# Kernel optimization log

Measured on AMD Instinct MI355X. Metric: run time of the kernel, lower is better.

The kernel has to match this reference:

```python
import jax, jax.numpy as jnp
import numpy as np

N_NODES = 100000
N_EDGES = 1600000
F_IN, HID, N_CLS = 64, 64, 40


def setup_inputs() -> dict:
    key = jax.random.key(0)
    ks = jax.random.split(key, 8)
    feats = jax.random.normal(ks[0], (N_NODES, F_IN), dtype=jnp.float32)
    src = jax.random.randint(ks[1], (N_EDGES,), 0, N_NODES, dtype=jnp.int32)
    dst = jax.random.randint(ks[2], (N_EDGES,), 0, N_NODES, dtype=jnp.int32)
    def lin(k, out_d, in_d):
        s = 1.0 / np.sqrt(in_d)
        return jax.random.uniform(k, (out_d, in_d), jnp.float32, -s, s)
    return {
        "features": feats,
        "src": src,
        "dst": dst,
        "W0": lin(ks[3], HID, F_IN), "b0": jnp.zeros((HID,), jnp.float32),
        "W1": lin(ks[4], HID, HID), "b1": jnp.zeros((HID,), jnp.float32),
        "W2": lin(ks[5], N_CLS, HID), "b2": jnp.zeros((N_CLS,), jnp.float32),
    }


def reference(features, src, dst, W0, b0, W1, b1, W2, b2):
    n = features.shape[0]
    # in-degrees (gcn aggregator normalizes by deg + 1, counting self-loop)
    deg = jax.ops.segment_sum(jnp.ones_like(dst, dtype=features.dtype), dst,
                              num_segments=n)  # [N]
    inv = 1.0 / (deg + 1.0)  # [N]

    def sage_gcn(h, W, b, act):
        # gather src features, sum into dst: message passing
        neigh = jax.ops.segment_sum(h[src], dst, num_segments=n)  # [N, d]
        h_neigh = (neigh + h) * inv[:, None]
        out = h_neigh @ W.T + b
        return jax.nn.relu(out) if act else out

    h = sage_gcn(features, W0, b0, True)
    h = sage_gcn(h, W1, b1, True)   # dropout = identity in eval mode
    h = sage_gcn(h, W2, b2, False)
    return h
```

## Files before the change

kernel.cpp:

```cpp
#include <hip/hip_runtime.h>
#include <hip/hip_bf16.h>


#define N_FEAT 64
#define CAP 64
#define CAPW 24
#define OVF_CAP 4096

__device__ __forceinline__ float rl(float v, int l) {
    return __int_as_float(__builtin_amdgcn_readlane(__float_as_int(v), l));
}

__device__ __forceinline__ void bin_body(const int* __restrict__ src,
                                         const int* __restrict__ dst,
                                         unsigned int* __restrict__ bins,
                                         unsigned long long* __restrict__ cnt64,
                                         int* __restrict__ ovf, int* __restrict__ ovf_cnt,
                                         int n_edges, int bsize, int nw, int bid) {
    const int e = bid * 256 + threadIdx.x;
    const int lane = threadIdx.x & 63;
    const int wid = (bid << 2) | (threadIdx.x >> 6);
    const bool valid = e < n_edges;
    int s = 0, d = 0;
    if (valid) { s = src[e]; d = dst[e]; }
    const unsigned int bucket = valid ? ((unsigned int)d / (unsigned int)bsize) : 8u;
    const unsigned int local = valid ? (unsigned int)(d - (int)bucket * bsize) : 0u;
    const unsigned int pack = (local << 17) | (unsigned int)s;

    int mycnt = 0;
    for (int c = 0; c < 8; ++c) {
        unsigned long long m = __ballot(valid && bucket == (unsigned int)c);
        int cc = __popcll(m);
        if (lane == c) mycnt = (cc < CAPW) ? cc : CAPW;
        if (valid && bucket == (unsigned int)c) {
            int pfx = __popcll(m & ((1ull << lane) - 1ull));
            if (pfx < CAPW) {
                __builtin_nontemporal_store(pack, &bins[((size_t)c * nw + wid) * CAPW + pfx]);
            } else {
                int p = atomicAdd(ovf_cnt, 1);
                if (p < OVF_CAP) { ovf[2 * p] = s; ovf[2 * p + 1] = d; }
            }
        }
    }
    unsigned long long packed = 0;
#pragma unroll
    for (int c = 0; c < 8; ++c) {
        int v = __builtin_amdgcn_readlane(mycnt, c);
        packed |= ((unsigned long long)(v & 0xFF)) << (8 * c);
    }
    if (lane == 0) cnt64[wid] = packed;
}

__device__ __forceinline__ void transform64_body(const float* __restrict__ h,
                                                 const float* __restrict__ W,
                                                 float* __restrict__ t, int n_nodes, int bid) {
    const int lane = threadIdx.x & 63;
    const int wave = (bid << 2) | (threadIdx.x >> 6);
    float4 wreg[16];
    const float4* W4 = (const float4*)(W + lane * N_FEAT);
#pragma unroll
    for (int k = 0; k < 16; ++k) wreg[k] = W4[k];
    const float* wf = (const float*)wreg;

    const int node0 = wave * 8;
    for (int k = 0; k < 8; ++k) {
        const int node = node0 + k;
        if (node >= n_nodes) return;
        const float hv = h[(size_t)node * N_FEAT + lane];
        float acc = 0.f;
#pragma unroll
        for (int f = 0; f < 64; ++f) acc = fmaf(rl(hv, f), wf[f], acc);
        t[(size_t)node * N_FEAT + lane] = acc;
    }
}

__global__ __launch_bounds__(256) void prep(const int* __restrict__ src,
                                            const int* __restrict__ dst,
                                            unsigned int* __restrict__ bins,
                                            unsigned long long* __restrict__ cnt64,
                                            int* __restrict__ ovf, int* __restrict__ ovf_cnt,
                                            int n_edges, int bsize, int nw,
                                            const float* __restrict__ feats,
                                            const float* __restrict__ W0,
                                            float* __restrict__ t0, int n_nodes, int PB) {
    const int b = (int)blockIdx.x;
    if (b < PB)
        bin_body(src, dst, bins, cnt64, ovf, ovf_cnt, n_edges, bsize, nw, b);
    else
        transform64_body(feats, W0, t0, n_nodes, b - PB);
}

__global__ __launch_bounds__(256) void fill_from_bins(const unsigned int* __restrict__ bins,
                                                      const unsigned long long* __restrict__ cnt64,
                                                      const int* __restrict__ ovf,
                                                      const int* __restrict__ ovf_cnt,
                                                      int* __restrict__ deg,
                                                      int* __restrict__ ell,
                                                      int nw, int bsize, int n_nodes) {
    const int lane = threadIdx.x & 63;
    const int w = threadIdx.x >> 6;
    const int c = blockIdx.x & 7;
    const int jb = blockIdx.x >> 3;
    const int base_node = c * bsize;
    const int sub = lane >> 3;
    const int rr = lane & 7;
    const int wave_in_bucket = jb * 4 + w;
    const int nwaves = (gridDim.x >> 3) * 4;
    const int shift = 8 * c;

    for (int s0 = wave_in_bucket * 8; s0 < nw; s0 += nwaves * 8) {
        const int sg = s0 + sub;
        unsigned long long word = (sg < nw) ? cnt64[sg] : 0ull;
        const int n = (int)((word >> shift) & 0xFFull);
#pragma unroll
        for (int t = 0; t < 3; ++t) {
            const int rec = t * 8 + rr;
            const bool act = rec < n;
            unsigned long long bm = __ballot(act);
            if (!bm) break;
            if (act) {
                unsigned int v = __builtin_nontemporal_load(
                    &bins[((size_t)c * nw + sg) * CAPW + rec]);
                int sv = (int)(v & 0x1FFFFu);
                int d = base_node + (int)(v >> 17);
                int slot = atomicAdd(&deg[d], 1);
                if (slot < CAP)
                    ell[(((size_t)(slot >> 4) * n_nodes + d) << 4) + (slot & 15)] = sv;
            }
        }
    }
    if (blockIdx.x == 0) {
        int n = *ovf_cnt; n = (n < OVF_CAP) ? n : OVF_CAP;
        for (int i = threadIdx.x; i < n; i += 256) {
            int sv = ovf[2 * i], d = ovf[2 * i + 1];
            int slot = atomicAdd(&deg[d], 1);
            if (slot < CAP)
                ell[(((size_t)(slot >> 4) * n_nodes + d) << 4) + (slot & 15)] = sv;
        }
    }
}

template <int OUTW, int NPW>
__global__ __launch_bounds__(256, 4) void agg_t_k(const float* __restrict__ t,
                                                  const float* __restrict__ bias,
                                                  const float* __restrict__ Wn,
                                                  const int* __restrict__ deg,
                                                  const int* __restrict__ ell,
                                                  float* __restrict__ tn,
                                                  int n_nodes) {
    __shared__ float4 sW[64 * 17];
    {
        const float4* Wg = (const float4*)Wn;
        for (int i = threadIdx.x; i < OUTW * 16; i += 256)
            sW[(i >> 4) * 17 + (i & 15)] = Wg[i];
    }
    __syncthreads();

    const int lane = threadIdx.x & 63;
    const int wave = (blockIdx.x << 2) | (threadIdx.x >> 6);
    const int g = lane >> 4;
    const int q = lane & 15;
    const float4* t4 = (const float4*)t;
    const int4* ell4 = (const int4*)ell;
    const float4 bq = ((const float4*)bias)[q];
    const int wrow = (OUTW == 64) ? lane : ((lane < OUTW) ? lane : 0);
    const float4* wrow4 = sW + wrow * 17;
    const bool has_out = (OUTW == 64) || (lane < OUTW);

    const int node0 = wave * NPW;
    if (node0 >= n_nodes) return;
    const int e0 = g * 4;

    if (node0 + NPW <= n_nodes) {
        int dg[NPW];
#pragma unroll
        for (int k = 0; k < NPW; ++k) dg[k] = deg[node0 + k];
        float4 self[NPW];
#pragma unroll
        for (int k = 0; k < NPW; ++k) self[k] = t4[(size_t)(node0 + k) * 16 + q];

        int4 idxb[2];
        float4 vb[2][4];
        idxb[0] = ell4[(size_t)node0 * 4 + g];
        {
            int4 ix = idxb[0]; const int d = dg[0];
            vb[0][0] = t4[(size_t)((e0 + 0 < d) ? ix.x : 0) * 16 + q];
            vb[0][1] = t4[(size_t)((e0 + 1 < d) ? ix.y : 0) * 16 + q];
            vb[0][2] = t4[(size_t)((e0 + 2 < d) ? ix.z : 0) * 16 + q];
            vb[0][3] = t4[(size_t)((e0 + 3 < d) ? ix.w : 0) * 16 + q];
        }
        if (NPW > 1) idxb[1] = ell4[(size_t)(node0 + 1) * 4 + g];

#pragma unroll
        for (int k = 0; k < NPW; ++k) {
            if (k + 1 < NPW) {
                int4 ix = idxb[(k + 1) & 1]; const int d = dg[k + 1];
                float4* v = vb[(k + 1) & 1];
                v[0] = t4[(size_t)((e0 + 0 < d) ? ix.x : 0) * 16 + q];
                v[1] = t4[(size_t)((e0 + 1 < d) ? ix.y : 0) * 16 + q];
                v[2] = t4[(size_t)((e0 + 2 < d) ? ix.z : 0) * 16 + q];
                v[3] = t4[(size_t)((e0 + 3 < d) ? ix.w : 0) * 16 + q];
            }
            if (k + 2 < NPW) idxb[k & 1] = ell4[(size_t)(node0 + k + 2) * 4 + g];

            const int node = node0 + k;
            const int d = dg[k];
            const float4* v = vb[k & 1];
            const float m0 = (e0 + 0 < d) ? 1.f : 0.f;
            const float m1 = (e0 + 1 < d) ? 1.f : 0.f;
            const float m2 = (e0 + 2 < d) ? 1.f : 0.f;
            const float m3 = (e0 + 3 < d) ? 1.f : 0.f;
            float4 acc;
            acc.x = m0 * v[0].x; acc.y = m0 * v[0].y; acc.z = m0 * v[0].z; acc.w = m0 * v[0].w;
            acc.x = fmaf(m1, v[1].x, acc.x); acc.y = fmaf(m1, v[1].y, acc.y);
            acc.z = fmaf(m1, v[1].z, acc.z); acc.w = fmaf(m1, v[1].w, acc.w);
            acc.x = fmaf(m2, v[2].x, acc.x); acc.y = fmaf(m2, v[2].y, acc.y);
            acc.z = fmaf(m2, v[2].z, acc.z); acc.w = fmaf(m2, v[2].w, acc.w);
            acc.x = fmaf(m3, v[3].x, acc.x); acc.y = fmaf(m3, v[3].y, acc.y);
            acc.z = fmaf(m3, v[3].z, acc.z); acc.w = fmaf(m3, v[3].w, acc.w);

            const int dcap = (d < CAP) ? d : CAP;
            for (int u = 1; u * 16 < dcap; ++u) {
                int4 ix = ell4[((size_t)u * n_nodes + node) * 4 + g];
                const int eb = u * 16 + g * 4;
                int i0 = (eb + 0 < d) ? ix.x : 0;
                int i1 = (eb + 1 < d) ? ix.y : 0;
                int i2 = (eb + 2 < d) ? ix.z : 0;
                int i3 = (eb + 3 < d) ? ix.w : 0;
                float n0 = (eb + 0 < d) ? 1.f : 0.f;
                float n1 = (eb + 1 < d) ? 1.f : 0.f;
                float n2 = (eb + 2 < d) ? 1.f : 0.f;
                float n3 = (eb + 3 < d) ? 1.f : 0.f;
                float4 w0 = t4[(size_t)i0 * 16 + q];
                float4 w1 = t4[(size_t)i1 * 16 + q];
                float4 w2 = t4[(size_t)i2 * 16 + q];
                float4 w3 = t4[(size_t)i3 * 16 + q];
                acc.x = fmaf(n0, w0.x, acc.x); acc.y = fmaf(n0, w0.y, acc.y);
                acc.z = fmaf(n0, w0.z, acc.z); acc.w = fmaf(n0, w0.w, acc.w);
                acc.x = fmaf(n1, w1.x, acc.x); acc.y = fmaf(n1, w1.y, acc.y);
                acc.z = fmaf(n1, w1.z, acc.z); acc.w = fmaf(n1, w1.w, acc.w);
                acc.x = fmaf(n2, w2.x, acc.x); acc.y = fmaf(n2, w2.y, acc.y);
                acc.z = fmaf(n2, w2.z, acc.z); acc.w = fmaf(n2, w2.w, acc.w);
                acc.x = fmaf(n3, w3.x, acc.x); acc.y = fmaf(n3, w3.y, acc.y);
                acc.z = fmaf(n3, w3.z, acc.z); acc.w = fmaf(n3, w3.w, acc.w);
            }

            acc.x += __shfl_xor(acc.x, 16, 64); acc.y += __shfl_xor(acc.y, 16, 64);
            acc.z += __shfl_xor(acc.z, 16, 64); acc.w += __shfl_xor(acc.w, 16, 64);
            acc.x += __shfl_xor(acc.x, 32, 64); acc.y += __shfl_xor(acc.y, 32, 64);
            acc.z += __shfl_xor(acc.z, 32, 64); acc.w += __shfl_xor(acc.w, 32, 64);

            const float invv = 1.0f / (float)(d + 1);
            float4 r;
            r.x = fmaxf((acc.x + self[k].x) * invv + bq.x, 0.f);
            r.y = fmaxf((acc.y + self[k].y) * invv + bq.y, 0.f);
            r.z = fmaxf((acc.z + self[k].z) * invv + bq.z, 0.f);
            r.w = fmaxf((acc.w + self[k].w) * invv + bq.w, 0.f);

            float o0 = 0.f, o1 = 0.f;
#pragma unroll
            for (int c = 0; c < 16; c += 2) {
                float4 w0 = wrow4[c];
                float4 w1 = wrow4[c + 1];
                o0 = fmaf(rl(r.x, c), w0.x, o0);
                o0 = fmaf(rl(r.y, c), w0.y, o0);
                o0 = fmaf(rl(r.z, c), w0.z, o0);
                o0 = fmaf(rl(r.w, c), w0.w, o0);
                o1 = fmaf(rl(r.x, c + 1), w1.x, o1);
                o1 = fmaf(rl(r.y, c + 1), w1.y, o1);
                o1 = fmaf(rl(r.z, c + 1), w1.z, o1);
                o1 = fmaf(rl(r.w, c + 1), w1.w, o1);
            }
            if (has_out) tn[(size_t)node * OUTW + lane] = o0 + o1;
        }
    } else {
        for (int k = 0; k < NPW; ++k) {
            const int node = node0 + k;
            if (node >= n_nodes) return;
            const int d = deg[node];
            const int dcap = (d < CAP) ? d : CAP;
            float4 acc = make_float4(0.f, 0.f, 0.f, 0.f);
            for (int u = 0; u * 16 < dcap; ++u) {
                int4 ix = ell4[((size_t)u * n_nodes + node) * 4 + g];
                const int eb = u * 16 + g * 4;
                for (int j = 0; j < 4; ++j) {
                    int ii = (j == 0) ? ix.x : (j == 1) ? ix.y : (j == 2) ? ix.z : ix.w;
                    float mm = (eb + j < d) ? 1.f : 0.f;
                    if (eb + j >= d) ii = 0;
                    float4 vv = t4[(size_t)ii * 16 + q];
                    acc.x = fmaf(mm, vv.x, acc.x); acc.y = fmaf(mm, vv.y, acc.y);
                    acc.z = fmaf(mm, vv.z, acc.z); acc.w = fmaf(mm, vv.w, acc.w);
                }
            }
            acc.x += __shfl_xor(acc.x, 16, 64); acc.y += __shfl_xor(acc.y, 16, 64);
            acc.z += __shfl_xor(acc.z, 16, 64); acc.w += __shfl_xor(acc.w, 16, 64);
            acc.x += __shfl_xor(acc.x, 32, 64); acc.y += __shfl_xor(acc.y, 32, 64);
            acc.z += __shfl_xor(acc.z, 32, 64); acc.w += __shfl_xor(acc.w, 32, 64);
            float4 self = t4[(size_t)node * 16 + q];
            const float invv = 1.0f / (float)(d + 1);
            float4 r;
            r.x = fmaxf((acc.x + self.x) * invv + bq.x, 0.f);
            r.y = fmaxf((acc.y + self.y) * invv + bq.y, 0.f);
            r.z = fmaxf((acc.z + self.z) * invv + bq.z, 0.f);
            r.w = fmaxf((acc.w + self.w) * invv + bq.w, 0.f);
            float o0 = 0.f, o1 = 0.f;
#pragma unroll
            for (int c = 0; c < 16; c += 2) {
                float4 w0 = wrow4[c];
                float4 w1 = wrow4[c + 1];
                o0 = fmaf(rl(r.x, c), w0.x, o0);
                o0 = fmaf(rl(r.y, c), w0.y, o0);
                o0 = fmaf(rl(r.z, c), w0.z, o0);
                o0 = fmaf(rl(r.w, c), w0.w, o0);
                o1 = fmaf(rl(r.x, c + 1), w1.x, o1);
                o1 = fmaf(rl(r.y, c + 1), w1.y, o1);
                o1 = fmaf(rl(r.z, c + 1), w1.z, o1);
                o1 = fmaf(rl(r.w, c + 1), w1.w, o1);
            }
            if (has_out) tn[(size_t)node * OUTW + lane] = o0 + o1;
        }
    }
}

template <int NPW>
__global__ __launch_bounds__(256) void agg40_k(const float* __restrict__ t,
                                               const float* __restrict__ bias,
                                               const int* __restrict__ deg,
                                               const int* __restrict__ ell,
                                               float* __restrict__ out, int n_nodes) {
    const int lane = threadIdx.x & 63;
    const int wave = (blockIdx.x << 2) | (threadIdx.x >> 6);
    const int g = lane / 10;
    const int q = lane - g * 10;
    const bool act = lane < 60;
    const float4* t4 = (const float4*)t;
    const float4 bq = ((const float4*)bias)[q];
    const int node0 = wave * NPW;
    if (node0 >= n_nodes) return;

    int nmax = NPW;
    if (node0 + NPW > n_nodes) nmax = n_nodes - node0;

    int dg[NPW];
#pragma unroll
    for (int k = 0; k < NPW; ++k) dg[k] = deg[node0 + ((k < nmax) ? k : 0)];

    auto eaddr = [&](int nd, int e) -> size_t {
        return (((size_t)(e >> 4) * n_nodes + nd) << 4) + (e & 15);
    };

    float4 vb[2][4];
    float mb[2][4];
    auto issue = [&](int slot, int k) {
        const int node = node0 + k;
        const int d = dg[k];
        const bool k0 = act && (g + 0 < d);
        const bool k1 = act && (g + 6 < d);
        const bool k2 = act && (g + 12 < d);
        const bool k3 = act && (g + 18 < d);
        int i0 = k0 ? ell[eaddr(node, g + 0)] : 0;
        int i1 = k1 ? ell[eaddr(node, g + 6)] : 0;
        int i2 = k2 ? ell[eaddr(node, g + 12)] : 0;
        int i3 = k3 ? ell[eaddr(node, g + 18)] : 0;
        vb[slot][0] = t4[(size_t)i0 * 10 + q];
        vb[slot][1] = t4[(size_t)i1 * 10 + q];
        vb[slot][2] = t4[(size_t)i2 * 10 + q];
        vb[slot][3] = t4[(size_t)i3 * 10 + q];
        mb[slot][0] = k0 ? 1.f : 0.f; mb[slot][1] = k1 ? 1.f : 0.f;
        mb[slot][2] = k2 ? 1.f : 0.f; mb[slot][3] = k3 ? 1.f : 0.f;
    };

    issue(0, 0);
#pragma unroll
    for (int k = 0; k < NPW; ++k) {
        if (k + 1 < NPW) issue((k + 1) & 1, k + 1);
        if (k >= nmax) break;
        const int node = node0 + k;
        const int d = dg[k];
        const float4* v = vb[k & 1];
        const float* m = mb[k & 1];
        float4 acc;
        acc.x = m[0] * v[0].x; acc.y = m[0] * v[0].y;
        acc.z = m[0] * v[0].z; acc.w = m[0] * v[0].w;
        acc.x = fmaf(m[1], v[1].x, acc.x); acc.y = fmaf(m[1], v[1].y, acc.y);
        acc.z = fmaf(m[1], v[1].z, acc.z); acc.w = fmaf(m[1], v[1].w, acc.w);
        acc.x = fmaf(m[2], v[2].x, acc.x); acc.y = fmaf(m[2], v[2].y, acc.y);
        acc.z = fmaf(m[2], v[2].z, acc.z); acc.w = fmaf(m[2], v[2].w, acc.w);
        acc.x = fmaf(m[3], v[3].x, acc.x); acc.y = fmaf(m[3], v[3].y, acc.y);
        acc.z = fmaf(m[3], v[3].z, acc.z); acc.w = fmaf(m[3], v[3].w, acc.w);

        const int dcap = (d < CAP) ? d : CAP;
        for (int u = 1; u * 24 < dcap; ++u) {
            const int eb = u * 24 + g;
            const bool k0 = act && (eb + 0 < d) && (eb + 0 < CAP);
            const bool k1 = act && (eb + 6 < d) && (eb + 6 < CAP);
            const bool k2 = act && (eb + 12 < d) && (eb + 12 < CAP);
            const bool k3 = act && (eb + 18 < d) && (eb + 18 < CAP);
            int i0 = k0 ? ell[eaddr(node, eb + 0)] : 0;
            int i1 = k1 ? ell[eaddr(node, eb + 6)] : 0;
            int i2 = k2 ? ell[eaddr(node, eb + 12)] : 0;
            int i3 = k3 ? ell[eaddr(node, eb + 18)] : 0;
            float n0 = k0 ? 1.f : 0.f;
            float n1 = k1 ? 1.f : 0.f;
            float n2 = k2 ? 1.f : 0.f;
            float n3 = k3 ? 1.f : 0.f;
            float4 w0 = t4[(size_t)i0 * 10 + q];
            float4 w1 = t4[(size_t)i1 * 10 + q];
            float4 w2 = t4[(size_t)i2 * 10 + q];
            float4 w3 = t4[(size_t)i3 * 10 + q];
            acc.x = fmaf(n0, w0.x, acc.x); acc.y = fmaf(n0, w0.y, acc.y);
            acc.z = fmaf(n0, w0.z, acc.z); acc.w = fmaf(n0, w0.w, acc.w);
            acc.x = fmaf(n1, w1.x, acc.x); acc.y = fmaf(n1, w1.y, acc.y);
            acc.z = fmaf(n1, w1.z, acc.z); acc.w = fmaf(n1, w1.w, acc.w);
            acc.x = fmaf(n2, w2.x, acc.x); acc.y = fmaf(n2, w2.y, acc.y);
            acc.z = fmaf(n2, w2.z, acc.z); acc.w = fmaf(n2, w2.w, acc.w);
            acc.x = fmaf(n3, w3.x, acc.x); acc.y = fmaf(n3, w3.y, acc.y);
            acc.z = fmaf(n3, w3.z, acc.z); acc.w = fmaf(n3, w3.w, acc.w);
        }

        acc.x += __shfl(acc.x, lane + 30, 64); acc.y += __shfl(acc.y, lane + 30, 64);
        acc.z += __shfl(acc.z, lane + 30, 64); acc.w += __shfl(acc.w, lane + 30, 64);
        float4 s1, s2;
        s1.x = __shfl(acc.x, lane + 10, 64); s2.x = __shfl(acc.x, lane + 20, 64);
        s1.y = __shfl(acc.y, lane + 10, 64); s2.y = __shfl(acc.y, lane + 20, 64);
        s1.z = __shfl(acc.z, lane + 10, 64); s2.z = __shfl(acc.z, lane + 20, 64);
        s1.w = __shfl(acc.w, lane + 10, 64); s2.w = __shfl(acc.w, lane + 20, 64);
        acc.x += s1.x + s2.x; acc.y += s1.y + s2.y;
        acc.z += s1.z + s2.z; acc.w += s1.w + s2.w;

        const float4 self = t4[(size_t)node * 10 + q];
        const float invv = 1.0f / (float)(d + 1);
        float4 r;
        r.x = (acc.x + self.x) * invv + bq.x;
        r.y = (acc.y + self.y) * invv + bq.y;
        r.z = (acc.z + self.z) * invv + bq.z;
        r.w = (acc.w + self.w) * invv + bq.w;
        if (lane < 10) ((float4*)out)[(size_t)node * 10 + q] = r;
    }
}

extern "C" void kernel_launch(void* const* d_in, const int* in_sizes, int n_in,
                              void* d_out, int out_size, void* d_ws, size_t ws_size,
                              hipStream_t stream) {
    const float* feats = (const float*)d_in[0];
    const int*   src   = (const int*)d_in[1];
    const int*   dst   = (const int*)d_in[2];
    const float* W0    = (const float*)d_in[3];
    const float* b0    = (const float*)d_in[4];
    const float* W1    = (const float*)d_in[5];
    const float* b1    = (const float*)d_in[6];
    const float* W2    = (const float*)d_in[7];
    const float* b2    = (const float*)d_in[8];
    float*       out   = (float*)d_out;

    const int N = in_sizes[0] / N_FEAT;
    const int E = in_sizes[1];
    const int PB = (E + 255) / 256;
    const int NW = PB * 4;
    const int BS = (N + 7) / 8;

    char* p = (char*)d_ws;
    float* X   = (float*)p; p += (size_t)N * N_FEAT * sizeof(float);
    float* Y   = (float*)p; p += (size_t)N * N_FEAT * sizeof(float);
    unsigned int* bins = (unsigned int*)Y;
    int*   deg = (int*)p;   p += (size_t)(N + 1) * sizeof(int);
    int*   ovf_cnt = deg + N;
    int*   ovf = (int*)p;   p += (size_t)OVF_CAP * 2 * sizeof(int);
    unsigned long long* cnt64 = (unsigned long long*)p;
    p += (size_t)NW * sizeof(unsigned long long);
    int*   ell = (int*)p;   p += (size_t)N * CAP * sizeof(int);

    hipMemsetAsync(deg, 0, (size_t)(N + 1) * sizeof(int), stream);

    constexpr int NPW = 4;
    const int tb = ((N + 7) / 8 + 3) / 4;
    const int ab = ((N + NPW - 1) / NPW + 3) / 4;

    prep<<<PB + tb, 256, 0, stream>>>(src, dst, bins, cnt64, ovf, ovf_cnt,
                                      E, BS, NW, feats, W0, X, N, PB);
    fill_from_bins<<<2048, 256, 0, stream>>>(bins, cnt64, ovf, ovf_cnt, deg, ell, NW, BS, N);
    agg_t_k<64, NPW><<<ab, 256, 0, stream>>>(X, b0, W1, deg, ell, Y, N);
    agg_t_k<40, NPW><<<ab, 256, 0, stream>>>(Y, b1, W2, deg, ell, X, N);
    agg40_k<NPW><<<ab, 256, 0, stream>>>(X, b2, deg, ell, out, N);
}
```

Before: 390.5 us.

## Pad ELL with sentinel zero row and widen slot chunks to 32

Pre-fills the ELL neighbor table with a sentinel index that points at an extra zeroed feature row, which removes per-edge masking and degree checks from the gathers. The ELL slot chunk grows from 16 to 32, so each node's first 32 neighbors come from one contiguous block, with at most one extra block for high-degree nodes. The sentinel fill is merged into the prep kernel. This trades extra memory writes for the init and some wasted gathers on padded slots against fewer conditionals and better load pipelining in the aggregation kernels.

```diff
diff --git a/kernel.cpp b/kernel.cpp
--- a/kernel.cpp
+++ b/kernel.cpp
@@ -74,6 +74,17 @@
     }
 }
 
+__device__ __forceinline__ void ell_init_body(int* __restrict__ ell,
+                                              float* __restrict__ xz,
+                                              int n_nodes, int bid, int nb) {
+    const size_t total4 = (size_t)n_nodes * (CAP / 4);
+    int4* e4 = (int4*)ell;
+    const int4 sv = make_int4(n_nodes, n_nodes, n_nodes, n_nodes);
+    for (size_t i = (size_t)bid * 256 + threadIdx.x; i < total4; i += (size_t)nb * 256)
+        e4[i] = sv;
+    if (bid == 0 && threadIdx.x < 64) xz[threadIdx.x] = 0.f;
+}
+
 __global__ __launch_bounds__(256) void prep(const int* __restrict__ src,
                                             const int* __restrict__ dst,
                                             unsigned int* __restrict__ bins,
@@ -82,12 +93,16 @@
                                             int n_edges, int bsize, int nw,
                                             const float* __restrict__ feats,
                                             const float* __restrict__ W0,
-                                            float* __restrict__ t0, int n_nodes, int PB) {
+                                            float* __restrict__ t0, int n_nodes,
+                                            int* __restrict__ ell,
+                                            int PB, int TB, int IB) {
     const int b = (int)blockIdx.x;
     if (b < PB)
         bin_body(src, dst, bins, cnt64, ovf, ovf_cnt, n_edges, bsize, nw, b);
+    else if (b < PB + TB)
+        transform64_body(feats, W0, t0, n_nodes, b - PB);
     else
-        transform64_body(feats, W0, t0, n_nodes, b - PB);
+        ell_init_body(ell, t0 + (size_t)n_nodes * N_FEAT, n_nodes, b - PB - TB, IB);
 }
 
 __global__ __launch_bounds__(256) void fill_from_bins(const unsigned int* __restrict__ bins,
@@ -125,7 +140,7 @@
                 int d = base_node + (int)(v >> 17);
                 int slot = atomicAdd(&deg[d], 1);
                 if (slot < CAP)
-                    ell[(((size_t)(slot >> 4) * n_nodes + d) << 4) + (slot & 15)] = sv;
+                    ell[(((size_t)(slot >> 5) * n_nodes + d) << 5) + (slot & 31)] = sv;
             }
         }
     }
@@ -135,7 +150,7 @@
             int sv = ovf[2 * i], d = ovf[2 * i + 1];
             int slot = atomicAdd(&deg[d], 1);
             if (slot < CAP)
-                ell[(((size_t)(slot >> 4) * n_nodes + d) << 4) + (slot & 15)] = sv;
+                ell[(((size_t)(slot >> 5) * n_nodes + d) << 5) + (slot & 31)] = sv;
         }
     }
 }
@@ -149,6 +164,8 @@
                                                   float* __restrict__ tn,
                                                   int n_nodes) {
     __shared__ float4 sW[64 * 17];
+    if (blockIdx.x == 0 && threadIdx.x < OUTW)
+        tn[(size_t)n_nodes * OUTW + threadIdx.x] = 0.f;
     {
         const float4* Wg = (const float4*)Wn;
         for (int i = threadIdx.x; i < OUTW * 16; i += 256)
@@ -157,10 +174,12 @@
     __syncthreads();
 
     const int lane = threadIdx.x & 63;
-    const int wave = (blockIdx.x << 2) | (threadIdx.x >> 6);
+    const int w = threadIdx.x >> 6;
+    const int wave = (blockIdx.x << 2) | w;
     const int g = lane >> 4;
     const int q = lane & 15;
     const float4* t4 = (const float4*)t;
+    const float4* tq = t4 + q;
     const int4* ell4 = (const int4*)ell;
     const float4 bq = ((const float4*)bias)[q];
     const int wrow = (OUTW == 64) ? lane : ((lane < OUTW) ? lane : 0);
@@ -169,80 +188,99 @@
 
     const int node0 = wave * NPW;
     if (node0 >= n_nodes) return;
-    const int e0 = g * 4;
+    const int gi = g * 2;
+
+#define GATH8(V, I)                         \
+    do {                                    \
+        V[0] = tq[(size_t)(I)[0].x * 16];   \
+        V[1] = tq[(size_t)(I)[0].y * 16];   \
+        V[2] = tq[(size_t)(I)[0].z * 16];   \
+        V[3] = tq[(size_t)(I)[0].w * 16];   \
+        V[4] = tq[(size_t)(I)[1].x * 16];   \
+        V[5] = tq[(size_t)(I)[1].y * 16];   \
+        V[6] = tq[(size_t)(I)[1].z * 16];   \
+        V[7] = tq[(size_t)(I)[1].w * 16];   \
+    } while (0)
+
+#define EPILOGUE_GEMM(R)                                  \
+    float o0 = 0.f, o1 = 0.f;                             \
+    _Pragma("unroll")                                     \
+    for (int c = 0; c < 16; c += 2) {                     \
+        float4 w0 = wrow4[c];                             \
+        float4 w1 = wrow4[c + 1];                         \
+        o0 = fmaf(rl((R).x, c), w0.x, o0);                \
+        o0 = fmaf(rl((R).y, c), w0.y, o0);                \
+        o0 = fmaf(rl((R).z, c), w0.z, o0);                \
+        o0 = fmaf(rl((R).w, c), w0.w, o0);                \
+        o1 = fmaf(rl((R).x, c + 1), w1.x, o1);            \
+        o1 = fmaf(rl((R).y, c + 1), w1.y, o1);            \
+        o1 = fmaf(rl((R).z, c + 1), w1.z, o1);            \
+        o1 = fmaf(rl((R).w, c + 1), w1.w, o1);            \
+    }
 
     if (node0 + NPW <= n_nodes) {
-        int dg[NPW];
-#pragma unroll
-        for (int k = 0; k < NPW; ++k) dg[k] = deg[node0 + k];
-        float4 self[NPW];
-#pragma unroll
-        for (int k = 0; k < NPW; ++k) self[k] = t4[(size_t)(node0 + k) * 16 + q];
-
-        int4 idxb[2];
-        float4 vb[2][4];
-        idxb[0] = ell4[(size_t)node0 * 4 + g];
-        {
-            int4 ix = idxb[0]; const int d = dg[0];
-            vb[0][0] = t4[(size_t)((e0 + 0 < d) ? ix.x : 0) * 16 + q];
-            vb[0][1] = t4[(size_t)((e0 + 1 < d) ? ix.y : 0) * 16 + q];
-            vb[0][2] = t4[(size_t)((e0 + 2 < d) ? ix.z : 0) * 16 + q];
-            vb[0][3] = t4[(size_t)((e0 + 3 < d) ? ix.w : 0) * 16 + q];
-        }
-        if (NPW > 1) idxb[1] = ell4[(size_t)(node0 + 1) * 4 + g];
+        int dgv[NPW];
+#pragma unroll
+        for (int k = 0; k < NPW; ++k) dgv[k] = deg[node0 + k];
+
+        int4 ix[2][2];
+        float4 vb[2][8];
+        float4 selfb[2];
+        ix[0][0] = ell4[(size_t)node0 * 8 + gi];
+        ix[0][1] = ell4[(size_t)node0 * 8 + gi + 1];
+        if (NPW > 1) {
+            ix[1][0] = ell4[(size_t)(node0 + 1) * 8 + gi];
+            ix[1][1] = ell4[(size_t)(node0 + 1) * 8 + gi + 1];
+        }
+        selfb[0] = t4[(size_t)node0 * 16 + q];
+        GATH8(vb[0], ix[0]);
 
 #pragma unroll
         for (int k = 0; k < NPW; ++k) {
             if (k + 1 < NPW) {
-                int4 ix = idxb[(k + 1) & 1]; const int d = dg[k + 1];
-                float4* v = vb[(k + 1) & 1];
-                v[0] = t4[(size_t)((e0 + 0 < d) ? ix.x : 0) * 16 + q];
-                v[1] = t4[(size_t)((e0 + 1 < d) ? ix.y : 0) * 16 + q];
-                v[2] = t4[(size_t)((e0 + 2 < d) ? ix.z : 0) * 16 + q];
-                v[3] = t4[(size_t)((e0 + 3 < d) ? ix.w : 0) * 16 + q];
-            }
-            if (k + 2 < NPW) idxb[k & 1] = ell4[(size_t)(node0 + k + 2) * 4 + g];
-
+                selfb[(k + 1) & 1] = t4[(size_t)(node0 + k + 1) * 16 + q];
+                GATH8(vb[(k + 1) & 1], ix[(k + 1) & 1]);
+            }
+            if (k + 2 < NPW) {
+                ix[k & 1][0] = ell4[(size_t)(node0 + k + 2) * 8 + gi];
+                ix[k & 1][1] = ell4[(size_t)(node0 + k + 2) * 8 + gi + 1];
+            }
             const int node = node0 + k;
-            const int d = dg[k];
+            const int d = dgv[k];
             const float4* v = vb[k & 1];
-            const float m0 = (e0 + 0 < d) ? 1.f : 0.f;
-            const float m1 = (e0 + 1 < d) ? 1.f : 0.f;
-            const float m2 = (e0 + 2 < d) ? 1.f : 0.f;
-            const float m3 = (e0 + 3 < d) ? 1.f : 0.f;
             float4 acc;
-            acc.x = m0 * v[0].x; acc.y = m0 * v[0].y; acc.z = m0 * v[0].z; acc.w = m0 * v[0].w;
-            acc.x = fmaf(m1, v[1].x, acc.x); acc.y = fmaf(m1, v[1].y, acc.y);
-            acc.z = fmaf(m1, v[1].z, acc.z); acc.w = fmaf(m1, v[1].w, acc.w);
-            acc.x = fmaf(m2, v[2].x, acc.x); acc.y = fmaf(m2, v[2].y, acc.y);
-            acc.z = fmaf(m2, v[2].z, acc.z); acc.w = fmaf(m2, v[2].w, acc.w);
-            acc.x = fmaf(m3, v[3].x, acc.x); acc.y = fmaf(m3, v[3].y, acc.y);
-            acc.z = fmaf(m3, v[3].z, acc.z); acc.w = fmaf(m3, v[3].w, acc.w);
-
-            const int dcap = (d < CAP) ? d : CAP;
-            for (int u = 1; u * 16 < dcap; ++u) {
-                int4 ix = ell4[((size_t)u * n_nodes + node) * 4 + g];
-                const int eb = u * 16 + g * 4;
-                int i0 = (eb + 0 < d) ? ix.x : 0;
-                int i1 = (eb + 1 < d) ? ix.y : 0;
-                int i2 = (eb + 2 < d) ? ix.z : 0;
-                int i3 = (eb + 3 < d) ? ix.w : 0;
-                float n0 = (eb + 0 < d) ? 1.f : 0.f;
-                float n1 = (eb + 1 < d) ? 1.f : 0.f;
-                float n2 = (eb + 2 < d) ? 1.f : 0.f;
-                float n3 = (eb + 3 < d) ? 1.f : 0.f;
-                float4 w0 = t4[(size_t)i0 * 16 + q];
-                float4 w1 = t4[(size_t)i1 * 16 + q];
-                float4 w2 = t4[(size_t)i2 * 16 + q];
-                float4 w3 = t4[(size_t)i3 * 16 + q];
-                acc.x = fmaf(n0, w0.x, acc.x); acc.y = fmaf(n0, w0.y, acc.y);
-                acc.z = fmaf(n0, w0.z, acc.z); acc.w = fmaf(n0, w0.w, acc.w);
-                acc.x = fmaf(n1, w1.x, acc.x); acc.y = fmaf(n1, w1.y, acc.y);
-                acc.z = fmaf(n1, w1.z, acc.z); acc.w = fmaf(n1, w1.w, acc.w);
-                acc.x = fmaf(n2, w2.x, acc.x); acc.y = fmaf(n2, w2.y, acc.y);
-                acc.z = fmaf(n2, w2.z, acc.z); acc.w = fmaf(n2, w2.w, acc.w);
-                acc.x = fmaf(n3, w3.x, acc.x); acc.y = fmaf(n3, w3.y, acc.y);
-                acc.z = fmaf(n3, w3.z, acc.z); acc.w = fmaf(n3, w3.w, acc.w);
+            acc.x = ((v[0].x + v[1].x) + (v[2].x + v[3].x)) +
+                    ((v[4].x + v[5].x) + (v[6].x + v[7].x));
+            acc.y = ((v[0].y + v[1].y) + (v[2].y + v[3].y)) +
+                    ((v[4].y + v[5].y) + (v[6].y + v[7].y));
+            acc.z = ((v[0].z + v[1].z) + (v[2].z + v[3].z)) +
+                    ((v[4].z + v[5].z) + (v[6].z + v[7].z));
+            acc.w = ((v[0].w + v[1].w) + (v[2].w + v[3].w)) +
+                    ((v[4].w + v[5].w) + (v[6].w + v[7].w));
+
+            if (d > 32) {
+                int4 j0 = ell4[((size_t)(n_nodes + node)) * 8 + gi];
+                int4 j1 = ell4[((size_t)(n_nodes + node)) * 8 + gi + 1];
+                {
+                    float4 u0 = tq[(size_t)j0.x * 16];
+                    float4 u1 = tq[(size_t)j0.y * 16];
+                    float4 u2 = tq[(size_t)j0.z * 16];
+                    float4 u3 = tq[(size_t)j0.w * 16];
+                    acc.x += (u0.x + u1.x) + (u2.x + u3.x);
+                    acc.y += (u0.y + u1.y) + (u2.y + u3.y);
+                    acc.z += (u0.z + u1.z) + (u2.z + u3.z);
+                    acc.w += (u0.w + u1.w) + (u2.w + u3.w);
+                }
+                {
+                    float4 u0 = tq[(size_t)j1.x * 16];
+                    float4 u1 = tq[(size_t)j1.y * 16];
+                    float4 u2 = tq[(size_t)j1.z * 16];
+                    float4 u3 = tq[(size_t)j1.w * 16];
+                    acc.x += (u0.x + u1.x) + (u2.x + u3.x);
+                    acc.y += (u0.y + u1.y) + (u2.y + u3.y);
+                    acc.z += (u0.z + u1.z) + (u2.z + u3.z);
+                    acc.w += (u0.w + u1.w) + (u2.w + u3.w);
+                }
             }
 
             acc.x += __shfl_xor(acc.x, 16, 64); acc.y += __shfl_xor(acc.y, 16, 64);
@@ -252,25 +290,12 @@
 
             const float invv = 1.0f / (float)(d + 1);
             float4 r;
-            r.x = fmaxf((acc.x + self[k].x) * invv + bq.x, 0.f);
-            r.y = fmaxf((acc.y + self[k].y) * invv + bq.y, 0.f);
-            r.z = fmaxf((acc.z + self[k].z) * invv + bq.z, 0.f);
-            r.w = fmaxf((acc.w + self[k].w) * invv + bq.w, 0.f);
-
-            float o0 = 0.f, o1 = 0.f;
-#pragma unroll
-            for (int c = 0; c < 16; c += 2) {
-                float4 w0 = wrow4[c];
-                float4 w1 = wrow4[c + 1];
-                o0 = fmaf(rl(r.x, c), w0.x, o0);
-                o0 = fmaf(rl(r.y, c), w0.y, o0);
-                o0 = fmaf(rl(r.z, c), w0.z, o0);
-                o0 = fmaf(rl(r.w, c), w0.w, o0);
-                o1 = fmaf(rl(r.x, c + 1), w1.x, o1);
-                o1 = fmaf(rl(r.y, c + 1), w1.y, o1);
-                o1 = fmaf(rl(r.z, c + 1), w1.z, o1);
-                o1 = fmaf(rl(r.w, c + 1), w1.w, o1);
-            }
+            r.x = fmaxf((acc.x + selfb[k & 1].x) * invv + bq.x, 0.f);
+            r.y = fmaxf((acc.y + selfb[k & 1].y) * invv + bq.y, 0.f);
+            r.z = fmaxf((acc.z + selfb[k & 1].z) * invv + bq.z, 0.f);
+            r.w = fmaxf((acc.w + selfb[k & 1].w) * invv + bq.w, 0.f);
+
+            EPILOGUE_GEMM(r);
             if (has_out) tn[(size_t)node * OUTW + lane] = o0 + o1;
         }
     } else {
@@ -278,19 +303,22 @@
             const int node = node0 + k;
             if (node >= n_nodes) return;
             const int d = deg[node];
-            const int dcap = (d < CAP) ? d : CAP;
             float4 acc = make_float4(0.f, 0.f, 0.f, 0.f);
-            for (int u = 0; u * 16 < dcap; ++u) {
-                int4 ix = ell4[((size_t)u * n_nodes + node) * 4 + g];
-                const int eb = u * 16 + g * 4;
-                for (int j = 0; j < 4; ++j) {
-                    int ii = (j == 0) ? ix.x : (j == 1) ? ix.y : (j == 2) ? ix.z : ix.w;
-                    float mm = (eb + j < d) ? 1.f : 0.f;
-                    if (eb + j >= d) ii = 0;
-                    float4 vv = t4[(size_t)ii * 16 + q];
-                    acc.x = fmaf(mm, vv.x, acc.x); acc.y = fmaf(mm, vv.y, acc.y);
-                    acc.z = fmaf(mm, vv.z, acc.z); acc.w = fmaf(mm, vv.w, acc.w);
-                }
+            const int np = (d > 32) ? 2 : 1;
+            for (int p = 0; p < np; ++p) {
+                int4 ii[2];
+                ii[0] = ell4[((size_t)p * n_nodes + node) * 8 + gi];
+                ii[1] = ell4[((size_t)p * n_nodes + node) * 8 + gi + 1];
+                float4 vv[8];
+                GATH8(vv, ii);
+                acc.x += ((vv[0].x + vv[1].x) + (vv[2].x + vv[3].x)) +
+                         ((vv[4].x + vv[5].x) + (vv[6].x + vv[7].x));
+                acc.y += ((vv[0].y + vv[1].y) + (vv[2].y + vv[3].y)) +
+                         ((vv[4].y + vv[5].y) + (vv[6].y + vv[7].y));
+                acc.z += ((vv[0].z + vv[1].z) + (vv[2].z + vv[3].z)) +
+                         ((vv[4].z + vv[5].z) + (vv[6].z + vv[7].z));
+                acc.w += ((vv[0].w + vv[1].w) + (vv[2].w + vv[3].w)) +
+                         ((vv[4].w + vv[5].w) + (vv[6].w + vv[7].w));
             }
             acc.x += __shfl_xor(acc.x, 16, 64); acc.y += __shfl_xor(acc.y, 16, 64);
             acc.z += __shfl_xor(acc.z, 16, 64); acc.w += __shfl_xor(acc.w, 16, 64);
@@ -303,23 +331,12 @@
             r.y = fmaxf((acc.y + self.y) * invv + bq.y, 0.f);
             r.z = fmaxf((acc.z + self.z) * invv + bq.z, 0.f);
             r.w = fmaxf((acc.w + self.w) * invv + bq.w, 0.f);
-            float o0 = 0.f, o1 = 0.f;
-#pragma unroll
-            for (int c = 0; c < 16; c += 2) {
-                float4 w0 = wrow4[c];
-                float4 w1 = wrow4[c + 1];
-                o0 = fmaf(rl(r.x, c), w0.x, o0);
-                o0 = fmaf(rl(r.y, c), w0.y, o0);
-                o0 = fmaf(rl(r.z, c), w0.z, o0);
-                o0 = fmaf(rl(r.w, c), w0.w, o0);
-                o1 = fmaf(rl(r.x, c + 1), w1.x, o1);
-                o1 = fmaf(rl(r.y, c + 1), w1.y, o1);
-                o1 = fmaf(rl(r.z, c + 1), w1.z, o1);
-                o1 = fmaf(rl(r.w, c + 1), w1.w, o1);
-            }
+            EPILOGUE_GEMM(r);
             if (has_out) tn[(size_t)node * OUTW + lane] = o0 + o1;
         }
     }
+#undef GATH8
+#undef EPILOGUE_GEMM
 }
 
 template <int NPW>
@@ -333,6 +350,7 @@
     const int g = lane / 10;
     const int q = lane - g * 10;
     const bool act = lane < 60;
+    const float actf = act ? 1.f : 0.f;
     const float4* t4 = (const float4*)t;
     const float4 bq = ((const float4*)bias)[q];
     const int node0 = wave * NPW;
@@ -346,28 +364,20 @@
     for (int k = 0; k < NPW; ++k) dg[k] = deg[node0 + ((k < nmax) ? k : 0)];
 
     auto eaddr = [&](int nd, int e) -> size_t {
-        return (((size_t)(e >> 4) * n_nodes + nd) << 4) + (e & 15);
+        return (((size_t)(e >> 5) * n_nodes + nd) << 5) + (e & 31);
     };
 
     float4 vb[2][4];
-    float mb[2][4];
     auto issue = [&](int slot, int k) {
         const int node = node0 + k;
-        const int d = dg[k];
-        const bool k0 = act && (g + 0 < d);
-        const bool k1 = act && (g + 6 < d);
-        const bool k2 = act && (g + 12 < d);
-        const bool k3 = act && (g + 18 < d);
-        int i0 = k0 ? ell[eaddr(node, g + 0)] : 0;
-        int i1 = k1 ? ell[eaddr(node, g + 6)] : 0;
-        int i2 = k2 ? ell[eaddr(node, g + 12)] : 0;
-        int i3 = k3 ? ell[eaddr(node, g + 18)] : 0;
+        int i0 = ell[eaddr(node, g + 0)];
+        int i1 = ell[eaddr(node, g + 6)];
+        int i2 = ell[eaddr(node, g + 12)];
+        int i3 = ell[eaddr(node, g + 18)];
         vb[slot][0] = t4[(size_t)i0 * 10 + q];
         vb[slot][1] = t4[(size_t)i1 * 10 + q];
         vb[slot][2] = t4[(size_t)i2 * 10 + q];
         vb[slot][3] = t4[(size_t)i3 * 10 + q];
-        mb[slot][0] = k0 ? 1.f : 0.f; mb[slot][1] = k1 ? 1.f : 0.f;
-        mb[slot][2] = k2 ? 1.f : 0.f; mb[slot][3] = k3 ? 1.f : 0.f;
     };
 
     issue(0, 0);
@@ -378,16 +388,11 @@
         const int node = node0 + k;
         const int d = dg[k];
         const float4* v = vb[k & 1];
-        const float* m = mb[k & 1];
         float4 acc;
-        acc.x = m[0] * v[0].x; acc.y = m[0] * v[0].y;
-        acc.z = m[0] * v[0].z; acc.w = m[0] * v[0].w;
-        acc.x = fmaf(m[1], v[1].x, acc.x); acc.y = fmaf(m[1], v[1].y, acc.y);
-        acc.z = fmaf(m[1], v[1].z, acc.z); acc.w = fmaf(m[1], v[1].w, acc.w);
-        acc.x = fmaf(m[2], v[2].x, acc.x); acc.y = fmaf(m[2], v[2].y, acc.y);
-        acc.z = fmaf(m[2], v[2].z, acc.z); acc.w = fmaf(m[2], v[2].w, acc.w);
-        acc.x = fmaf(m[3], v[3].x, acc.x); acc.y = fmaf(m[3], v[3].y, acc.y);
-        acc.z = fmaf(m[3], v[3].z, acc.z); acc.w = fmaf(m[3], v[3].w, acc.w);
+        acc.x = (v[0].x + v[1].x) + (v[2].x + v[3].x);
+        acc.y = (v[0].y + v[1].y) + (v[2].y + v[3].y);
+        acc.z = (v[0].z + v[1].z) + (v[2].z + v[3].z);
+        acc.w = (v[0].w + v[1].w) + (v[2].w + v[3].w);
 
         const int dcap = (d < CAP) ? d : CAP;
         for (int u = 1; u * 24 < dcap; ++u) {
@@ -396,28 +401,21 @@
             const bool k1 = act && (eb + 6 < d) && (eb + 6 < CAP);
             const bool k2 = act && (eb + 12 < d) && (eb + 12 < CAP);
             const bool k3 = act && (eb + 18 < d) && (eb + 18 < CAP);
-            int i0 = k0 ? ell[eaddr(node, eb + 0)] : 0;
-            int i1 = k1 ? ell[eaddr(node, eb + 6)] : 0;
-            int i2 = k2 ? ell[eaddr(node, eb + 12)] : 0;
-            int i3 = k3 ? ell[eaddr(node, eb + 18)] : 0;
-            float n0 = k0 ? 1.f : 0.f;
-            float n1 = k1 ? 1.f : 0.f;
-            float n2 = k2 ? 1.f : 0.f;
-            float n3 = k3 ? 1.f : 0.f;
+            int i0 = k0 ? ell[eaddr(node, eb + 0)] : n_nodes;
+            int i1 = k1 ? ell[eaddr(node, eb + 6)] : n_nodes;
+            int i2 = k2 ? ell[eaddr(node, eb + 12)] : n_nodes;
+            int i3 = k3 ? ell[eaddr(node, eb + 18)] : n_nodes;
             float4 w0 = t4[(size_t)i0 * 10 + q];
             float4 w1 = t4[(size_t)i1 * 10 + q];
             float4 w2 = t4[(size_t)i2 * 10 + q];
             float4 w3 = t4[(size_t)i3 * 10 + q];
-            acc.x = fmaf(n0, w0.x, acc.x); acc.y = fmaf(n0, w0.y, acc.y);
-            acc.z = fmaf(n0, w0.z, acc.z); acc.w = fmaf(n0, w0.w, acc.w);
-            acc.x = fmaf(n1, w1.x, acc.x); acc.y = fmaf(n1, w1.y, acc.y);
-            acc.z = fmaf(n1, w1.z, acc.z); acc.w = fmaf(n1, w1.w, acc.w);
-            acc.x = fmaf(n2, w2.x, acc.x); acc.y = fmaf(n2, w2.y, acc.y);
-            acc.z = fmaf(n2, w2.z, acc.z); acc.w = fmaf(n2, w2.w, acc.w);
-            acc.x = fmaf(n3, w3.x, acc.x); acc.y = fmaf(n3, w3.y, acc.y);
-            acc.z = fmaf(n3, w3.z, acc.z); acc.w = fmaf(n3, w3.w, acc.w);
-        }
-
+            acc.x += (w0.x + w1.x) + (w2.x + w3.x);
+            acc.y += (w0.y + w1.y) + (w2.y + w3.y);
+            acc.z += (w0.z + w1.z) + (w2.z + w3.z);
+            acc.w += (w0.w + w1.w) + (w2.w + w3.w);
+        }
+
+        acc.x *= actf; acc.y *= actf; acc.z *= actf; acc.w *= actf;
         acc.x += __shfl(acc.x, lane + 30, 64); acc.y += __shfl(acc.y, lane + 30, 64);
         acc.z += __shfl(acc.z, lane + 30, 64); acc.w += __shfl(acc.w, lane + 30, 64);
         float4 s1, s2;
@@ -460,10 +458,10 @@
     const int BS = (N + 7) / 8;
 
     char* p = (char*)d_ws;
-    float* X   = (float*)p; p += (size_t)N * N_FEAT * sizeof(float);
-    float* Y   = (float*)p; p += (size_t)N * N_FEAT * sizeof(float);
+    float* X   = (float*)p; p += ((size_t)N * N_FEAT + 64) * sizeof(float);
+    float* Y   = (float*)p; p += ((size_t)N * N_FEAT + 64) * sizeof(float);
     unsigned int* bins = (unsigned int*)Y;
-    int*   deg = (int*)p;   p += (size_t)(N + 1) * sizeof(int);
+    int*   deg = (int*)p;   p += (size_t)(N + 4) * sizeof(int);
     int*   ovf_cnt = deg + N;
     int*   ovf = (int*)p;   p += (size_t)OVF_CAP * 2 * sizeof(int);
     unsigned long long* cnt64 = (unsigned long long*)p;
@@ -473,11 +471,12 @@
     hipMemsetAsync(deg, 0, (size_t)(N + 1) * sizeof(int), stream);
 
     constexpr int NPW = 4;
-    const int tb = ((N + 7) / 8 + 3) / 4;
+    const int TB = ((N + 7) / 8 + 3) / 4;
+    const int IB = 1024;
     const int ab = ((N + NPW - 1) / NPW + 3) / 4;
 
-    prep<<<PB + tb, 256, 0, stream>>>(src, dst, bins, cnt64, ovf, ovf_cnt,
-                                      E, BS, NW, feats, W0, X, N, PB);
+    prep<<<PB + TB + IB, 256, 0, stream>>>(src, dst, bins, cnt64, ovf, ovf_cnt,
+                                           E, BS, NW, feats, W0, X, N, ell, PB, TB, IB);
     fill_from_bins<<<2048, 256, 0, stream>>>(bins, cnt64, ovf, ovf_cnt, deg, ell, NW, BS, N);
     agg_t_k<64, NPW><<<ab, 256, 0, stream>>>(X, b0, W1, deg, ell, Y, N);
     agg_t_k<40, NPW><<<ab, 256, 0, stream>>>(Y, b1, W2, deg, ell, X, N);
```

Measured after the change: 384.9 us. Within noise of the previous version (-1.4%).
